# Kernel tuning notes

Hardware: AMD Instinct MI355X
Metric: run time of the kernel (lower is better)

The kernel has to match this reference:

```python
import jax, jax.numpy as jnp
import numpy as np

NU, NI, E, C, L, B = 100000, 50000, 500000, 128, 2, 1024
EPS = 1e-5


def setup_inputs() -> dict:
    key = jax.random.key(0)
    ks = jax.random.split(key, 9)
    s = 1.0 / np.sqrt(C)
    return {
        "x_user": jax.random.normal(ks[0], (NU, C), jnp.float32),
        "x_item": jax.random.normal(ks[1], (NI, C), jnp.float32),
        "e_ui_src": jax.random.randint(ks[2], (E,), 0, NU, dtype=jnp.int32),
        "e_ui_dst": jax.random.randint(ks[3], (E,), 0, NI, dtype=jnp.int32),
        "e_iu_src": jax.random.randint(ks[4], (E,), 0, NI, dtype=jnp.int32),
        "e_iu_dst": jax.random.randint(ks[5], (E,), 0, NU, dtype=jnp.int32),
        "w_rel": jax.random.normal(ks[6], (L, 2, C, C), jnp.float32) * s,   # [layer, edge_type(ui,iu), C_in, C_out]
        "w_root": jax.random.normal(ks[7], (L, 2, C, C), jnp.float32) * s,
        "b": jnp.zeros((L, 2, C), jnp.float32),
        "ln_g": jnp.ones((L, 2, C), jnp.float32),   # [layer, node_type(user,item), C]
        "ln_b": jnp.zeros((L, 2, C), jnp.float32),
        "lin_w": jax.random.normal(ks[8], (C, 1), jnp.float32) * s,
        "lin_b": jnp.zeros((1,), jnp.float32),
    }


def _layer_norm(x, g, beta):
    # LayerNorm(mode='node'): normalize each node's feature vector
    mu = jnp.mean(x, axis=-1, keepdims=True)
    var = jnp.var(x, axis=-1, keepdims=True)
    return (x - mu) * jax.lax.rsqrt(var + EPS) * g + beta


def reference(x_user, x_item, e_ui_src, e_ui_dst, e_iu_src, e_iu_dst,
              w_rel, w_root, b, ln_g, ln_b, lin_w, lin_b):
    xu, xi = x_user, x_item
    for l in range(L):
        # GraphConv per edge type: lin_rel(sum-aggregated neighbor feats) + lin_root(x_dst) + bias
        agg_i = jax.ops.segment_sum(xu[e_ui_src], e_ui_dst, num_segments=NI)  # user -> item
        agg_u = jax.ops.segment_sum(xi[e_iu_src], e_iu_dst, num_segments=NU)  # item -> user
        out_i = agg_i @ w_rel[l, 0] + xi @ w_root[l, 0] + b[l, 0]
        out_u = agg_u @ w_rel[l, 1] + xu @ w_root[l, 1] + b[l, 1]
        # per-node-type LayerNorm + ReLU (dropout is identity in eval)
        xu = jax.nn.relu(_layer_norm(out_u, ln_g[l, 0], ln_b[l, 0]))
        xi = jax.nn.relu(_layer_norm(out_i, ln_g[l, 1], ln_b[l, 1]))
    # final head on the B seed nodes of the entity table ('user')
    return xu[:B] @ lin_w + lin_b
```

## Files before the change

### kernel.cpp

```cpp
#include <hip/hip_runtime.h>
#include <stdint.h>

static constexpr int kNU = 100000;
static constexpr int kNI = 50000;
static constexpr int kE  = 500000;
static constexpr int kC  = 128;
static constexpr int kB  = 1024;
static constexpr int kNBK = 256;
static constexpr int kCap = 4096;

typedef __attribute__((ext_vector_type(8))) short bf16x8;
typedef __attribute__((ext_vector_type(4))) float f32x4;

__device__ __forceinline__ unsigned short f2bf(float f) {
  unsigned u = __float_as_uint(f);
  unsigned r = (u + 0x7fffu + ((u >> 16) & 1u)) >> 16;
  return (unsigned short)r;
}

__device__ __forceinline__ void gload_lds16(const unsigned short* g, unsigned short* l) {
  __builtin_amdgcn_global_load_lds(
      (const __attribute__((address_space(1))) unsigned int*)g,
      (__attribute__((address_space(3))) unsigned int*)l, 16, 0, 0);
}

__global__ void cvt_kernel(const float* __restrict__ xu, const float* __restrict__ xi,
                           unsigned short* __restrict__ fu0, unsigned short* __restrict__ fu1,
                           unsigned short* __restrict__ fi0, unsigned short* __restrict__ fi1) {
  int i = blockIdx.x * blockDim.x + threadIdx.x;
  const int nu4 = kNU * kC / 4;
  const int ni4 = kNI * kC / 4;
  if (i < nu4) {
    float4 v = ((const float4*)xu)[i];
    ushort4 o; o.x = f2bf(v.x); o.y = f2bf(v.y); o.z = f2bf(v.z); o.w = f2bf(v.w);
    ((ushort4*)fu0)[i] = o;
  } else if (i < nu4 + ni4) {
    int j = i - nu4;
    float4 v = ((const float4*)xi)[j];
    ushort4 o; o.x = f2bf(v.x); o.y = f2bf(v.y); o.z = f2bf(v.z); o.w = f2bf(v.w);
    ((ushort4*)fi0)[j] = o;
  } else {
    int j = i - nu4 - ni4;
    if (j < 128) {
      int w = j >> 5;
      int o = j & 31;
      unsigned short* dst = (w == 0) ? fu0 + (size_t)kNU * kC
                          : (w == 1) ? fu1 + (size_t)kNU * kC
                          : (w == 2) ? fi0 + (size_t)kNI * kC
                                     : fi1 + (size_t)kNI * kC;
      ushort4 z; z.x = 0; z.y = 0; z.z = 0; z.w = 0;
      ((ushort4*)dst)[o] = z;
    }
  }
}

__global__ void prep_w_kernel(const float* __restrict__ wrel, const float* __restrict__ wroot,
                              unsigned short* __restrict__ wcat) {
  int id = blockIdx.x * 256 + threadIdx.x;
  int m = id >> 15;
  int n = (id >> 8) & 127;
  int k = id & 255;
  float v = (k < 128) ? wrel[(m * 128 + k) * 128 + n] : wroot[(m * 128 + (k - 128)) * 128 + n];
  wcat[id] = f2bf(v);
}

__global__ void binA_kernel(const int* __restrict__ dst_i, const int* __restrict__ dst_u,
                            int* __restrict__ bh_i, int* __restrict__ bh_u) {
  __shared__ int h[256];
  int b = blockIdx.x;
  const int* dst;
  int shift;
  int* bh;
  int blk;
  if (b < kNBK) { dst = dst_i; shift = 8; bh = bh_i; blk = b; }
  else          { dst = dst_u; shift = 9; bh = bh_u; blk = b - kNBK; }
  int tid = threadIdx.x;
  h[tid] = 0;
  __syncthreads();
  int chunk = (kE + kNBK - 1) / kNBK;
  int beg = blk * chunk;
  int end = min(kE, beg + chunk);
  for (int i = beg + tid; i < end; i += 256) atomicAdd(&h[dst[i] >> shift], 1);
  __syncthreads();
  bh[blk * 256 + tid] = h[tid];
}

__global__ void binB_kernel(const int* __restrict__ bh_i, int* __restrict__ bo_i,
                            int* __restrict__ base_i, const int* __restrict__ bh_u,
                            int* __restrict__ bo_u, int* __restrict__ base_u) {
  __shared__ int s[256];
  const int* bh;
  int* bo;
  int* base;
  if (blockIdx.x == 0) { bh = bh_i; bo = bo_i; base = base_i; }
  else                 { bh = bh_u; bo = bo_u; base = base_u; }
  int t = threadIdx.x;
  int run = 0;
  for (int b = 0; b < kNBK; ++b) {
    int v = bh[b * 256 + t];
    bo[b * 256 + t] = run;
    run += v;
  }
  s[t] = run;
  __syncthreads();
  for (int m = 1; m < 256; m <<= 1) {
    int tv = 0;
    if (t >= m) tv = s[t - m];
    __syncthreads();
    s[t] += tv;
    __syncthreads();
  }
  base[t] = s[t] - run;
  if (t == 255) base[256] = s[255];
}

__global__ void binC_kernel(const int* __restrict__ src_i, const int* __restrict__ dst_i,
                            const int* __restrict__ bo_i, const int* __restrict__ base_i,
                            unsigned* __restrict__ packed_i, const int* __restrict__ src_u,
                            const int* __restrict__ dst_u, const int* __restrict__ bo_u,
                            const int* __restrict__ base_u, unsigned* __restrict__ packed_u) {
  __shared__ int cur[256];
  int b = blockIdx.x;
  const int *src, *dst, *bo, *base;
  unsigned* packed;
  int shift, blk;
  if (b < kNBK) { src = src_i; dst = dst_i; bo = bo_i; base = base_i; packed = packed_i; shift = 8; blk = b; }
  else          { src = src_u; dst = dst_u; bo = bo_u; base = base_u; packed = packed_u; shift = 9; blk = b - kNBK; }
  int tid = threadIdx.x;
  cur[tid] = base[tid] + bo[blk * 256 + tid];
  __syncthreads();
  int chunk = (kE + kNBK - 1) / kNBK;
  int beg = blk * chunk;
  int end = min(kE, beg + chunk);
  int mask = (1 << shift) - 1;
  for (int i = beg + tid; i < end; i += 256) {
    int d = dst[i];
    int p = atomicAdd(&cur[d >> shift], 1);
    packed[p] = (unsigned)src[i] | ((unsigned)(d & mask) << 17);
  }
}

__launch_bounds__(256)
__global__ void binD_kernel(const unsigned* __restrict__ packed_i, const int* __restrict__ base_i,
                            int* __restrict__ col_i, int* __restrict__ rowptr_i,
                            const unsigned* __restrict__ packed_u, const int* __restrict__ base_u,
                            int* __restrict__ col_u, int* __restrict__ rowptr_u) {
  __shared__ unsigned ent[kCap];
  __shared__ int srt[kCap];
  __shared__ int hist[512];
  __shared__ int cur[512];
  int b = blockIdx.x;
  const unsigned* packed;
  const int* base;
  int* col;
  int* rowptr;
  int bsize, Nd, bb;
  if (b < 196) { packed = packed_i; base = base_i; col = col_i; rowptr = rowptr_i; bsize = 256; Nd = kNI; bb = b; }
  else         { packed = packed_u; base = base_u; col = col_u; rowptr = rowptr_u; bsize = 512; Nd = kNU; bb = b - 196; }
  int tid = threadIdx.x;
  int seg_beg = base[bb], seg_end = base[bb + 1];
  int cnt = seg_end - seg_beg;
  if (cnt > kCap) cnt = kCap;
  hist[tid] = 0;
  hist[tid + 256] = 0;
  __syncthreads();
  for (int i = tid; i < cnt; i += 256) {
    unsigned e = packed[seg_beg + i];
    ent[i] = e;
    atomicAdd(&hist[e >> 17], 1);
  }
  __syncthreads();
  for (int d = 1; d < 512; d <<= 1) {
    int idx = (tid + 1) * 2 * d - 1;
    if (idx < 512) hist[idx] += hist[idx - d];
    __syncthreads();
  }
  if (tid == 0) hist[511] = 0;
  __syncthreads();
  for (int d = 256; d >= 1; d >>= 1) {
    int idx = (tid + 1) * 2 * d - 1;
    if (idx < 512) {
      int tmp = hist[idx - d];
      hist[idx - d] = hist[idx];
      hist[idx] += tmp;
    }
    __syncthreads();
  }
  for (int j = tid; j < bsize; j += 256) {
    int n = bb * bsize + j;
    if (n < Nd) rowptr[n] = seg_beg + hist[j];
  }
  if (bb == 195 && tid == 0) rowptr[Nd] = seg_end;
  cur[tid] = hist[tid];
  cur[tid + 256] = hist[tid + 256];
  __syncthreads();
  for (int i = tid; i < cnt; i += 256) {
    unsigned e = ent[i];
    int p = atomicAdd(&cur[e >> 17], 1);
    srt[p] = (int)(e & 0x1FFFFu);
  }
  __syncthreads();
  for (int i = tid; i < cnt; i += 256) col[seg_beg + i] = srt[i];
}

__global__ void pull4_kernel(const int* __restrict__ rp_i, const int* __restrict__ col_i,
                             const unsigned short* __restrict__ ft_i, unsigned short* __restrict__ ag_i,
                             const int* __restrict__ rp_u, const int* __restrict__ col_u,
                             const unsigned short* __restrict__ ft_u, unsigned short* __restrict__ ag_u,
                             int nbi) {
  int b = blockIdx.x;
  const int *rowptr, *col;
  const unsigned short* feat;
  unsigned short* agg;
  int Nd, rbase, NZ;
  if (b < nbi) { rowptr = rp_i; col = col_i; feat = ft_i; agg = ag_i; Nd = kNI; rbase = b * 16; NZ = kNU; }
  else         { rowptr = rp_u; col = col_u; feat = ft_u; agg = ag_u; Nd = kNU; rbase = (b - nbi) * 16; NZ = kNI; }
  int tid = threadIdx.x;
  int wv = tid >> 6;
  int lane = tid & 63;
  int qrow = lane >> 4;
  int qoff = lane & 15;
  int r = rbase + wv * 4 + qrow;
  int beg = 0, end = 0;
  if (r < Nd) {
    beg = rowptr[r];
    end = rowptr[r + 1];
  }
  float acc[8];
#pragma unroll
  for (int c = 0; c < 8; ++c) acc[c] = 0.f;

  int idx[8];
#pragma unroll
  for (int i = 0; i < 8; ++i) idx[i] = (beg + i < end) ? col[beg + i] : NZ;

  int choff = qoff * 8;
  for (int j = beg; j < end; j += 8) {
    int nxt[8];
#pragma unroll
    for (int i = 0; i < 8; ++i) {
      int jj = j + 8 + i;
      nxt[i] = (jj < end) ? col[jj] : NZ;
    }
    uint4 g0 = *(const uint4*)(feat + (size_t)idx[0] * kC + choff);
    uint4 g1 = *(const uint4*)(feat + (size_t)idx[1] * kC + choff);
    uint4 g2 = *(const uint4*)(feat + (size_t)idx[2] * kC + choff);
    uint4 g3 = *(const uint4*)(feat + (size_t)idx[3] * kC + choff);
    uint4 g4 = *(const uint4*)(feat + (size_t)idx[4] * kC + choff);
    uint4 g5 = *(const uint4*)(feat + (size_t)idx[5] * kC + choff);
    uint4 g6 = *(const uint4*)(feat + (size_t)idx[6] * kC + choff);
    uint4 g7 = *(const uint4*)(feat + (size_t)idx[7] * kC + choff);
#define ACC8(g)                                          \
    acc[0] += __uint_as_float((g).x << 16);              \
    acc[1] += __uint_as_float((g).x & 0xffff0000u);      \
    acc[2] += __uint_as_float((g).y << 16);              \
    acc[3] += __uint_as_float((g).y & 0xffff0000u);      \
    acc[4] += __uint_as_float((g).z << 16);              \
    acc[5] += __uint_as_float((g).z & 0xffff0000u);      \
    acc[6] += __uint_as_float((g).w << 16);              \
    acc[7] += __uint_as_float((g).w & 0xffff0000u);
    ACC8(g0)
    ACC8(g1)
    ACC8(g2)
    ACC8(g3)
    ACC8(g4)
    ACC8(g5)
    ACC8(g6)
    ACC8(g7)
#undef ACC8
#pragma unroll
    for (int i = 0; i < 8; ++i) idx[i] = nxt[i];
  }
  if (r < Nd) {
    uint4 o;
    o.x = (unsigned)f2bf(acc[0]) | ((unsigned)f2bf(acc[1]) << 16);
    o.y = (unsigned)f2bf(acc[2]) | ((unsigned)f2bf(acc[3]) << 16);
    o.z = (unsigned)f2bf(acc[4]) | ((unsigned)f2bf(acc[5]) << 16);
    o.w = (unsigned)f2bf(acc[6]) | ((unsigned)f2bf(acc[7]) << 16);
    *(uint4*)(agg + (size_t)r * kC + choff) = o;
  }
}

__launch_bounds__(256, 4)
__global__ void gemm10_kernel(int nbi,
                              const unsigned short* __restrict__ ag_i, const unsigned short* __restrict__ ft_i,
                              const unsigned short* __restrict__ wc_i, const float* __restrict__ bs_i,
                              const float* __restrict__ gm_i, const float* __restrict__ bt_i,
                              unsigned short* __restrict__ out_i,
                              const unsigned short* __restrict__ ag_u, const unsigned short* __restrict__ ft_u,
                              const unsigned short* __restrict__ wc_u, const float* __restrict__ bs_u,
                              const float* __restrict__ gm_u, const float* __restrict__ bt_u,
                              unsigned short* __restrict__ out_u) {
  __shared__ __attribute__((aligned(16))) unsigned short Ws[128 * 128];
  int b = blockIdx.x;
  const unsigned short *agg, *feat, *wcat;
  const float *bias, *gamma, *beta;
  unsigned short* out;
  int N, row0;
  if (b < nbi) {
    agg = ag_i; feat = ft_i; wcat = wc_i; bias = bs_i; gamma = gm_i; beta = bt_i; out = out_i;
    N = kNI; row0 = b * 128;
  } else {
    agg = ag_u; feat = ft_u; wcat = wc_u; bias = bs_u; gamma = gm_u; beta = bt_u; out = out_u;
    N = kNU; row0 = (b - nbi) * 128;
  }
  int tid = threadIdx.x;
  int lane = tid & 63;
  int wv = tid >> 6;
  int q = lane >> 4;
  int c0 = lane & 15;

  {
    int p0 = lane & 15;
    int rsub = lane >> 4;
#pragma unroll
    for (int o = 0; o < 8; ++o) {
      int n = wv * 32 + o * 4 + rsub;
      int j = p0 ^ (n & 7);
      gload_lds16(wcat + n * 256 + j * 8, &Ws[(wv * 32 + o * 4) * 128]);
    }
  }

  int rs = row0 + wv * 32;
  size_t baseA = (size_t)(rs + c0) * kC;
  size_t baseB = (size_t)(rs + 16 + c0) * kC;
  bf16x8 aA[4], aB[4];
#pragma unroll
  for (int ks = 0; ks < 4; ++ks) {
    aA[ks] = *(const bf16x8*)(agg + baseA + ks * 32 + q * 8);
    aB[ks] = *(const bf16x8*)(agg + baseB + ks * 32 + q * 8);
  }
  f32x4 accA[8], accB[8];
#pragma unroll
  for (int nt = 0; nt < 8; ++nt) {
    accA[nt] = (f32x4){0.f, 0.f, 0.f, 0.f};
    accB[nt] = (f32x4){0.f, 0.f, 0.f, 0.f};
  }
  asm volatile("s_waitcnt vmcnt(0)" ::: "memory");
  __syncthreads();

  int rsw = c0 & 7;
#pragma unroll
  for (int ks = 0; ks < 4; ++ks) {
    int chp = ((ks * 4 + q) ^ rsw) * 8;
#pragma unroll
    for (int nt = 0; nt < 8; ++nt) {
      bf16x8 bfr = *(const bf16x8*)&Ws[(nt * 16 + c0) * 128 + chp];
      accA[nt] = __builtin_amdgcn_mfma_f32_16x16x32_bf16(aA[ks], bfr, accA[nt], 0, 0, 0);
      accB[nt] = __builtin_amdgcn_mfma_f32_16x16x32_bf16(aB[ks], bfr, accB[nt], 0, 0, 0);
    }
    aA[ks] = *(const bf16x8*)(feat + baseA + ks * 32 + q * 8);
    aB[ks] = *(const bf16x8*)(feat + baseB + ks * 32 + q * 8);
  }

  __syncthreads();
  {
    int p0 = lane & 15;
    int rsub = lane >> 4;
#pragma unroll
    for (int o = 0; o < 8; ++o) {
      int n = wv * 32 + o * 4 + rsub;
      int j = p0 ^ (n & 7);
      gload_lds16(wcat + n * 256 + 128 + j * 8, &Ws[(wv * 32 + o * 4) * 128]);
    }
  }
  asm volatile("s_waitcnt vmcnt(0)" ::: "memory");
  __syncthreads();

#pragma unroll
  for (int ks = 0; ks < 4; ++ks) {
    int chp = ((ks * 4 + q) ^ rsw) * 8;
#pragma unroll
    for (int nt = 0; nt < 8; ++nt) {
      bf16x8 bfr = *(const bf16x8*)&Ws[(nt * 16 + c0) * 128 + chp];
      accA[nt] = __builtin_amdgcn_mfma_f32_16x16x32_bf16(aA[ks], bfr, accA[nt], 0, 0, 0);
      accB[nt] = __builtin_amdgcn_mfma_f32_16x16x32_bf16(aB[ks], bfr, accB[nt], 0, 0, 0);
    }
  }

  float bcol[8], gcol[8], ecol[8];
#pragma unroll
  for (int nt = 0; nt < 8; ++nt) {
    bcol[nt] = bias[nt * 16 + c0];
    gcol[nt] = gamma[nt * 16 + c0];
    ecol[nt] = beta[nt * 16 + c0];
  }

#pragma unroll
  for (int half = 0; half < 2; ++half) {
    int rbh = rs + half * 16;
#pragma unroll
    for (int reg = 0; reg < 4; ++reg) {
      int row = rbh + q * 4 + reg;
      float v[8];
      float s1 = 0.f, s2 = 0.f;
#pragma unroll
      for (int nt = 0; nt < 8; ++nt) {
        float t = (half ? accB[nt][reg] : accA[nt][reg]) + bcol[nt];
        v[nt] = t;
        s1 += t;
        s2 += t * t;
      }
#pragma unroll
      for (int m = 1; m < 16; m <<= 1) {
        s1 += __shfl_xor(s1, m, 64);
        s2 += __shfl_xor(s2, m, 64);
      }
      float mu = s1 * (1.f / 128.f);
      float var = s2 * (1.f / 128.f) - mu * mu;
      float rsq = rsqrtf(var + 1e-5f);
      if (row < N) {
#pragma unroll
        for (int nt = 0; nt < 8; ++nt) {
          float o = fmaxf((v[nt] - mu) * rsq * gcol[nt] + ecol[nt], 0.f);
          unsigned short h = f2bf(o);
          unsigned up = __shfl_xor((unsigned)h, 1, 64);
          if ((lane & 1) == 0) {
            *(unsigned*)(out + (size_t)row * kC + nt * 16 + c0) = (unsigned)h | (up << 16);
          }
        }
      }
    }
  }
}

__global__ void head_kernel(const unsigned short* __restrict__ fu, const float* __restrict__ lw,
                            const float* __restrict__ lb, float* __restrict__ out) {
  int w = (blockIdx.x * blockDim.x + threadIdx.x) >> 6;
  int lane = threadIdx.x & 63;
  if (w >= kB) return;
  unsigned v = *(const unsigned*)(fu + w * kC + lane * 2);
  float2 ww = *(const float2*)(lw + lane * 2);
  float p = __uint_as_float(v << 16) * ww.x + __uint_as_float(v & 0xffff0000u) * ww.y;
#pragma unroll
  for (int m = 1; m < 64; m <<= 1) p += __shfl_xor(p, m, 64);
  if (lane == 0) out[w] = p + lb[0];
}

extern "C" void kernel_launch(void* const* d_in, const int* in_sizes, int n_in,
                              void* d_out, int out_size, void* d_ws, size_t ws_size,
                              hipStream_t stream) {
  const float* x_user = (const float*)d_in[0];
  const float* x_item = (const float*)d_in[1];
  const int* e_ui_src = (const int*)d_in[2];
  const int* e_ui_dst = (const int*)d_in[3];
  const int* e_iu_src = (const int*)d_in[4];
  const int* e_iu_dst = (const int*)d_in[5];
  const float* w_rel  = (const float*)d_in[6];
  const float* w_root = (const float*)d_in[7];
  const float* bvec   = (const float*)d_in[8];
  const float* ln_g   = (const float*)d_in[9];
  const float* ln_b   = (const float*)d_in[10];
  const float* lin_w  = (const float*)d_in[11];
  const float* lin_b  = (const float*)d_in[12];

  char* p = (char*)d_ws;
  auto carve = [&](size_t bytes) -> char* {
    char* r = p;
    p += (bytes + 255) & ~size_t(255);
    return r;
  };
  unsigned short* fu[2] = {(unsigned short*)carve((size_t)(kNU + 1) * kC * 2),
                           (unsigned short*)carve((size_t)(kNU + 1) * kC * 2)};
  unsigned short* fi[2] = {(unsigned short*)carve((size_t)(kNI + 1) * kC * 2),
                           (unsigned short*)carve((size_t)(kNI + 1) * kC * 2)};
  unsigned short* agg_i = (unsigned short*)carve((size_t)kNI * kC * 2);
  unsigned short* agg_u = (unsigned short*)carve((size_t)kNU * kC * 2);
  unsigned short* wcat  = (unsigned short*)carve((size_t)4 * 128 * 256 * 2);
  int* bh_i   = (int*)carve((size_t)kNBK * 256 * 4);
  int* bo_i   = (int*)carve((size_t)kNBK * 256 * 4);
  int* bh_u   = (int*)carve((size_t)kNBK * 256 * 4);
  int* bo_u   = (int*)carve((size_t)kNBK * 256 * 4);
  int* base_i = (int*)carve(257 * 4);
  int* base_u = (int*)carve(257 * 4);
  unsigned* packed_i = (unsigned*)carve((size_t)kE * 4);
  unsigned* packed_u = (unsigned*)carve((size_t)kE * 4);
  int* col_i    = (int*)carve((size_t)(kE + 4) * 4);
  int* col_u    = (int*)carve((size_t)(kE + 4) * 4);
  int* rowptr_i = (int*)carve((size_t)(kNI + 1) * 4);
  int* rowptr_u = (int*)carve((size_t)(kNU + 1) * 4);

  int cvtN = (kNU * kC + kNI * kC) / 4 + 128;
  cvt_kernel<<<(cvtN + 255) / 256, 256, 0, stream>>>(x_user, x_item, fu[0], fu[1], fi[0], fi[1]);
  prep_w_kernel<<<512, 256, 0, stream>>>(w_rel, w_root, wcat);

  binA_kernel<<<2 * kNBK, 256, 0, stream>>>(e_ui_dst, e_iu_dst, bh_i, bh_u);
  binB_kernel<<<2, 256, 0, stream>>>(bh_i, bo_i, base_i, bh_u, bo_u, base_u);
  binC_kernel<<<2 * kNBK, 256, 0, stream>>>(e_ui_src, e_ui_dst, bo_i, base_i, packed_i,
                                            e_iu_src, e_iu_dst, bo_u, base_u, packed_u);
  binD_kernel<<<392, 256, 0, stream>>>(packed_i, base_i, col_i, rowptr_i,
                                       packed_u, base_u, col_u, rowptr_u);

  int nbi_p = (kNI + 15) / 16;
  int nbi_g = (kNI + 127) / 128;
  int nbu_pB = kB / 16;
  int nbu_gB = kB / 128;

  pull4_kernel<<<nbi_p + nbu_pB, 256, 0, stream>>>(rowptr_i, col_i, fu[0], agg_i,
                                                   rowptr_u, col_u, fi[0], agg_u, nbi_p);
  gemm10_kernel<<<nbi_g + nbu_gB, 256, 0, stream>>>(
      nbi_g,
      agg_i, fi[0], wcat + (size_t)0 * 128 * 256,
      bvec + (size_t)0 * kC, ln_g + (size_t)1 * kC, ln_b + (size_t)1 * kC, fi[1],
      agg_u, fu[0], wcat + (size_t)1 * 128 * 256,
      bvec + (size_t)1 * kC, ln_g + (size_t)0 * kC, ln_b + (size_t)0 * kC, fu[1]);

  pull4_kernel<<<nbu_pB, 256, 0, stream>>>(rowptr_i, col_i, fu[1], agg_i,
                                           rowptr_u, col_u, fi[1], agg_u, 0);
  gemm10_kernel<<<nbu_gB, 256, 0, stream>>>(
      0,
      agg_i, fi[1], wcat + (size_t)2 * 128 * 256,
      bvec + (size_t)2 * kC, ln_g + (size_t)3 * kC, ln_b + (size_t)3 * kC, fi[0],
      agg_u, fu[1], wcat + (size_t)3 * 128 * 256,
      bvec + (size_t)3 * kC, ln_g + (size_t)2 * kC, ln_b + (size_t)2 * kC, fu[0]);

  head_kernel<<<(kB + 3) / 4, 256, 0, stream>>>(fu[0], lin_w, lin_b, (float*)d_out);
}
```

Before: 228.6 us.

## Restrict layer-one item updates to items feeding the seed users

Adds mark, compact and init kernels that build a compacted list of the item nodes that are sources of edges into the first B users. The layer-one item pull and GEMM then process only those items, indexed through the list, instead of all NI items. Only those items are read by the layer-two seed-user aggregation, so the skipped rows are never used. This trades three small extra kernels, an atomic compaction and indirect indexing for a large cut in layer-one item work.

```diff
diff --git a/kernel.cpp b/kernel.cpp
--- a/kernel.cpp
+++ b/kernel.cpp
@@ -64,6 +64,32 @@
   wcat[id] = f2bf(v);
 }
 
+__global__ void needinit_kernel(unsigned* __restrict__ mark, int* __restrict__ rlist,
+                                int* __restrict__ cnt) {
+  int i = blockIdx.x * 256 + threadIdx.x;
+  if (i < (kNI + 31) / 32) mark[i] = 0;
+  if (i < kNI + 128) rlist[i] = kNI;
+  if (i == 0) *cnt = 0;
+}
+
+__global__ void mark_kernel(const int* __restrict__ src, const int* __restrict__ dst,
+                            unsigned* __restrict__ mark) {
+  int i = blockIdx.x * 256 + threadIdx.x;
+  if (i < kE && dst[i] < kB) {
+    int it = src[i];
+    atomicOr(&mark[it >> 5], 1u << (it & 31));
+  }
+}
+
+__global__ void compact_kernel(const unsigned* __restrict__ mark, int* __restrict__ rlist,
+                               int* __restrict__ cnt) {
+  int i = blockIdx.x * 256 + threadIdx.x;
+  if (i < kNI && ((mark[i >> 5] >> (i & 31)) & 1u)) {
+    int p = atomicAdd(cnt, 1);
+    rlist[p] = i;
+  }
+}
+
 __global__ void binA_kernel(const int* __restrict__ dst_i, const int* __restrict__ dst_u,
                             int* __restrict__ bh_i, int* __restrict__ bh_u) {
   __shared__ int h[256];
@@ -203,26 +229,32 @@
   for (int i = tid; i < cnt; i += 256) col[seg_beg + i] = srt[i];
 }
 
-__global__ void pull4_kernel(const int* __restrict__ rp_i, const int* __restrict__ col_i,
+__global__ void pull5_kernel(const int* __restrict__ rp_i, const int* __restrict__ col_i,
                              const unsigned short* __restrict__ ft_i, unsigned short* __restrict__ ag_i,
                              const int* __restrict__ rp_u, const int* __restrict__ col_u,
                              const unsigned short* __restrict__ ft_u, unsigned short* __restrict__ ag_u,
+                             const int* __restrict__ rlist, const int* __restrict__ pcnt,
                              int nbi) {
   int b = blockIdx.x;
+  bool ind = (b < nbi);
   const int *rowptr, *col;
   const unsigned short* feat;
   unsigned short* agg;
   int Nd, rbase, NZ;
-  if (b < nbi) { rowptr = rp_i; col = col_i; feat = ft_i; agg = ag_i; Nd = kNI; rbase = b * 16; NZ = kNU; }
-  else         { rowptr = rp_u; col = col_u; feat = ft_u; agg = ag_u; Nd = kNU; rbase = (b - nbi) * 16; NZ = kNI; }
+  if (ind) { rowptr = rp_i; col = col_i; feat = ft_i; agg = ag_i; Nd = kNI; rbase = b * 16; NZ = kNU; }
+  else     { rowptr = rp_u; col = col_u; feat = ft_u; agg = ag_u; Nd = kNU; rbase = (b - nbi) * 16; NZ = kNI; }
+  int cnt = ind ? *pcnt : Nd;
+  if (rbase >= cnt) return;
   int tid = threadIdx.x;
   int wv = tid >> 6;
   int lane = tid & 63;
   int qrow = lane >> 4;
   int qoff = lane & 15;
-  int r = rbase + wv * 4 + qrow;
+  int slot = rbase + wv * 4 + qrow;
+  bool valid = slot < cnt;
   int beg = 0, end = 0;
-  if (r < Nd) {
+  if (valid) {
+    int r = ind ? rlist[slot] : slot;
     beg = rowptr[r];
     end = rowptr[r + 1];
   }
@@ -271,18 +303,18 @@
 #pragma unroll
     for (int i = 0; i < 8; ++i) idx[i] = nxt[i];
   }
-  if (r < Nd) {
+  if (valid) {
     uint4 o;
     o.x = (unsigned)f2bf(acc[0]) | ((unsigned)f2bf(acc[1]) << 16);
     o.y = (unsigned)f2bf(acc[2]) | ((unsigned)f2bf(acc[3]) << 16);
     o.z = (unsigned)f2bf(acc[4]) | ((unsigned)f2bf(acc[5]) << 16);
     o.w = (unsigned)f2bf(acc[6]) | ((unsigned)f2bf(acc[7]) << 16);
-    *(uint4*)(agg + (size_t)r * kC + choff) = o;
+    *(uint4*)(agg + (size_t)slot * kC + choff) = o;
   }
 }
 
 __launch_bounds__(256, 4)
-__global__ void gemm10_kernel(int nbi,
+__global__ void gemm11_kernel(int nbi, const int* __restrict__ rlist, const int* __restrict__ pcnt,
                               const unsigned short* __restrict__ ag_i, const unsigned short* __restrict__ ft_i,
                               const unsigned short* __restrict__ wc_i, const float* __restrict__ bs_i,
                               const float* __restrict__ gm_i, const float* __restrict__ bt_i,
@@ -293,17 +325,20 @@
                               unsigned short* __restrict__ out_u) {
   __shared__ __attribute__((aligned(16))) unsigned short Ws[128 * 128];
   int b = blockIdx.x;
+  bool ind = (b < nbi);
   const unsigned short *agg, *feat, *wcat;
   const float *bias, *gamma, *beta;
   unsigned short* out;
   int N, row0;
-  if (b < nbi) {
+  if (ind) {
     agg = ag_i; feat = ft_i; wcat = wc_i; bias = bs_i; gamma = gm_i; beta = bt_i; out = out_i;
     N = kNI; row0 = b * 128;
   } else {
     agg = ag_u; feat = ft_u; wcat = wc_u; bias = bs_u; gamma = gm_u; beta = bt_u; out = out_u;
     N = kNU; row0 = (b - nbi) * 128;
   }
+  int cnt = ind ? *pcnt : N;
+  if (row0 >= cnt) return;
   int tid = threadIdx.x;
   int lane = tid & 63;
   int wv = tid >> 6;
@@ -322,13 +357,19 @@
   }
 
   int rs = row0 + wv * 32;
-  size_t baseA = (size_t)(rs + c0) * kC;
-  size_t baseB = (size_t)(rs + 16 + c0) * kC;
+  int slotA = rs + c0;
+  int slotB = rs + 16 + c0;
+  int rowAf = ind ? ((slotA < cnt) ? rlist[slotA] : kNI) : slotA;
+  int rowBf = ind ? ((slotB < cnt) ? rlist[slotB] : kNI) : slotB;
+  size_t baseAa = (size_t)slotA * kC;
+  size_t baseBa = (size_t)slotB * kC;
+  size_t baseAf = (size_t)rowAf * kC;
+  size_t baseBf = (size_t)rowBf * kC;
   bf16x8 aA[4], aB[4];
 #pragma unroll
   for (int ks = 0; ks < 4; ++ks) {
-    aA[ks] = *(const bf16x8*)(agg + baseA + ks * 32 + q * 8);
-    aB[ks] = *(const bf16x8*)(agg + baseB + ks * 32 + q * 8);
+    aA[ks] = *(const bf16x8*)(agg + baseAa + ks * 32 + q * 8);
+    aB[ks] = *(const bf16x8*)(agg + baseBa + ks * 32 + q * 8);
   }
   f32x4 accA[8], accB[8];
 #pragma unroll
@@ -349,8 +390,8 @@
       accA[nt] = __builtin_amdgcn_mfma_f32_16x16x32_bf16(aA[ks], bfr, accA[nt], 0, 0, 0);
       accB[nt] = __builtin_amdgcn_mfma_f32_16x16x32_bf16(aB[ks], bfr, accB[nt], 0, 0, 0);
     }
-    aA[ks] = *(const bf16x8*)(feat + baseA + ks * 32 + q * 8);
-    aB[ks] = *(const bf16x8*)(feat + baseB + ks * 32 + q * 8);
+    aA[ks] = *(const bf16x8*)(feat + baseAf + ks * 32 + q * 8);
+    aB[ks] = *(const bf16x8*)(feat + baseBf + ks * 32 + q * 8);
   }
 
   __syncthreads();
@@ -388,10 +429,10 @@
 
 #pragma unroll
   for (int half = 0; half < 2; ++half) {
-    int rbh = rs + half * 16;
+    int sbh = rs + half * 16;
 #pragma unroll
     for (int reg = 0; reg < 4; ++reg) {
-      int row = rbh + q * 4 + reg;
+      int slot_r = sbh + q * 4 + reg;
       float v[8];
       float s1 = 0.f, s2 = 0.f;
 #pragma unroll
@@ -409,6 +450,7 @@
       float mu = s1 * (1.f / 128.f);
       float var = s2 * (1.f / 128.f) - mu * mu;
       float rsq = rsqrtf(var + 1e-5f);
+      int row = ind ? ((slot_r < cnt) ? rlist[slot_r] : N) : slot_r;
       if (row < N) {
 #pragma unroll
         for (int nt = 0; nt < 8; ++nt) {
@@ -479,10 +521,17 @@
   int* col_u    = (int*)carve((size_t)(kE + 4) * 4);
   int* rowptr_i = (int*)carve((size_t)(kNI + 1) * 4);
   int* rowptr_u = (int*)carve((size_t)(kNU + 1) * 4);
+  unsigned* mark = (unsigned*)carve(((kNI + 31) / 32) * 4);
+  int* rlist = (int*)carve((size_t)(kNI + 128) * 4);
+  int* cntp  = (int*)carve(4);
 
   int cvtN = (kNU * kC + kNI * kC) / 4 + 128;
   cvt_kernel<<<(cvtN + 255) / 256, 256, 0, stream>>>(x_user, x_item, fu[0], fu[1], fi[0], fi[1]);
   prep_w_kernel<<<512, 256, 0, stream>>>(w_rel, w_root, wcat);
+
+  needinit_kernel<<<(kNI + 128 + 255) / 256, 256, 0, stream>>>(mark, rlist, cntp);
+  mark_kernel<<<(kE + 255) / 256, 256, 0, stream>>>(e_iu_src, e_iu_dst, mark);
+  compact_kernel<<<(kNI + 255) / 256, 256, 0, stream>>>(mark, rlist, cntp);
 
   binA_kernel<<<2 * kNBK, 256, 0, stream>>>(e_ui_dst, e_iu_dst, bh_i, bh_u);
   binB_kernel<<<2, 256, 0, stream>>>(bh_i, bo_i, base_i, bh_u, bo_u, base_u);
@@ -496,19 +545,21 @@
   int nbu_pB = kB / 16;
   int nbu_gB = kB / 128;
 
-  pull4_kernel<<<nbi_p + nbu_pB, 256, 0, stream>>>(rowptr_i, col_i, fu[0], agg_i,
-                                                   rowptr_u, col_u, fi[0], agg_u, nbi_p);
-  gemm10_kernel<<<nbi_g + nbu_gB, 256, 0, stream>>>(
-      nbi_g,
+  pull5_kernel<<<nbi_p + nbu_pB, 256, 0, stream>>>(rowptr_i, col_i, fu[0], agg_i,
+                                                   rowptr_u, col_u, fi[0], agg_u,
+                                                   rlist, cntp, nbi_p);
+  gemm11_kernel<<<nbi_g + nbu_gB, 256, 0, stream>>>(
+      nbi_g, rlist, cntp,
       agg_i, fi[0], wcat + (size_t)0 * 128 * 256,
       bvec + (size_t)0 * kC, ln_g + (size_t)1 * kC, ln_b + (size_t)1 * kC, fi[1],
       agg_u, fu[0], wcat + (size_t)1 * 128 * 256,
       bvec + (size_t)1 * kC, ln_g + (size_t)0 * kC, ln_b + (size_t)0 * kC, fu[1]);
 
-  pull4_kernel<<<nbu_pB, 256, 0, stream>>>(rowptr_i, col_i, fu[1], agg_i,
-                                           rowptr_u, col_u, fi[1], agg_u, 0);
-  gemm10_kernel<<<nbu_gB, 256, 0, stream>>>(
-      0,
+  pull5_kernel<<<nbu_pB, 256, 0, stream>>>(rowptr_i, col_i, fu[1], agg_i,
+                                           rowptr_u, col_u, fi[1], agg_u,
+                                           rlist, cntp, 0);
+  gemm11_kernel<<<nbu_gB, 256, 0, stream>>>(
+      0, rlist, cntp,
       agg_i, fi[1], wcat + (size_t)2 * 128 * 256,
       bvec + (size_t)2 * kC, ln_g + (size_t)3 * kC, ln_b + (size_t)3 * kC, fi[0],
       agg_u, fu[1], wcat + (size_t)3 * 128 * 256,
```

Result: no change. 226.0 us (-1.1%).
